# Optimization experiments

Measured on AMD Instinct MI355X. Metric: run time of the kernel, lower is better.

Reference implementation:

```python
import jax, jax.numpy as jnp
import numpy as np
from jax import lax

B, T, H, CTX, CONV_OUT = 32, 1536, 1024, 1024, 32


def setup_inputs() -> dict:
    key = jax.random.key(0)
    ks = jax.random.split(key, 10)
    s = 1.0 / np.sqrt(H)
    return {
        "decoder_output": jax.random.normal(ks[0], (B, 1, H), jnp.float32),
        "encoder_outputs": jax.random.normal(ks[1], (B, T, H), jnp.float32),
        "last_alignment": jax.random.uniform(ks[2], (B, T), jnp.float32),
        "W": jax.random.normal(ks[3], (CTX, H), jnp.float32) * s,
        "V": jax.random.normal(ks[4], (CTX, H), jnp.float32) * s,
        "U": jax.random.normal(ks[5], (CTX, CONV_OUT), jnp.float32) * (1.0 / np.sqrt(CONV_OUT)),
        "b": jax.random.uniform(ks[6], (CTX,), jnp.float32, -0.1, 0.1),
        "w": jax.random.normal(ks[7], (CTX,), jnp.float32) * (1.0 / np.sqrt(CTX)),
        "conv_w": jax.random.normal(ks[8], (CONV_OUT, 1, 3), jnp.float32) * 0.5,
        "conv_b": jax.random.normal(ks[9], (CONV_OUT,), jnp.float32) * 0.1,
    }


def reference(decoder_output, encoder_outputs, last_alignment, W, V, U, b, w, conv_w, conv_b):
    # location feature: Conv1d(1 -> conv_out, k=3, pad=1) over previous alignment
    conv = lax.conv_general_dilated(
        last_alignment[:, None, :], conv_w,
        window_strides=(1,), padding=[(1, 1)],
        dimension_numbers=("NCW", "OIW", "NCW"),
    ) + conv_b[None, :, None]                      # (B, conv_out, T)
    loc = jnp.transpose(conv, (0, 2, 1))           # (B, T, conv_out)

    # additive (Bahdanau) energies: (B,1,ctx) + (B,T,ctx) + (B,T,ctx) + (ctx,)
    e = jnp.tanh(
        jnp.einsum("bqh,ch->bqc", decoder_output, W)
        + jnp.einsum("bth,ch->btc", encoder_outputs, V)
        + jnp.einsum("btk,ck->btc", loc, U)
        + b
    )                                              # (B, T, ctx)
    scores = jnp.einsum("btc,c->bt", e, w)         # (B, T)
    alignment = jax.nn.softmax(scores, axis=-1)    # (B, T)
    context = jnp.einsum("bt,bth->bh", alignment, encoder_outputs)  # (B, H)
    return context, alignment
```

## Files before the change

kernel.cpp:

```cpp
#include <hip/hip_runtime.h>
#include <hip/hip_bf16.h>
#include <hip/hip_fp16.h>


constexpr int kB = 32, kT = 1536, kH = 1024, kC = 1024, kCO = 32;
constexpr int kM = kB * kT;
constexpr int kKp = 1088;

typedef _Float16 f16;
typedef _Float16 f16x8 __attribute__((ext_vector_type(8)));
typedef float f32x4 __attribute__((ext_vector_type(4)));

constexpr size_t W2_A    = 0;
constexpr size_t W2_B    = W2_A + (size_t)kM * kKp * 2;
constexpr size_t W2_ADD  = W2_B + (size_t)kC * kKp * 2;
constexpr size_t W2_SCR  = W2_ADD + (size_t)kB * kC * 4;

__device__ __forceinline__ void gload16(const void* g, void* l) {
    __builtin_amdgcn_global_load_lds(
        (const __attribute__((address_space(1))) void*)g,
        (__attribute__((address_space(3))) void*)l, 16, 0, 0);
}

__global__ void k_cvt(const float* __restrict__ enc, f16* __restrict__ Af) {
    int gid = blockIdx.x * 256 + threadIdx.x;
    int row = gid >> 7, c8 = gid & 127;
    const float* src = enc + (size_t)row * kH + c8 * 8;
    float4 e0 = *(const float4*)src;
    float4 e1 = *(const float4*)(src + 4);
    union { f16 h[8]; int4 q; } u;
    u.h[0] = (f16)e0.x; u.h[1] = (f16)e0.y; u.h[2] = (f16)e0.z; u.h[3] = (f16)e0.w;
    u.h[4] = (f16)e1.x; u.h[5] = (f16)e1.y; u.h[6] = (f16)e1.z; u.h[7] = (f16)e1.w;
    *(int4*)(Af + (size_t)row * kKp + c8 * 8) = u.q;
}

__global__ void k_loc(const float* __restrict__ la, const float* __restrict__ cw,
                      const float* __restrict__ cb, f16* __restrict__ Af) {
    int m = blockIdx.x * 256 + threadIdx.x;
    int b = m / kT, t = m - b * kT;
    float x0 = (t > 0)      ? la[(size_t)b * kT + t - 1] : 0.f;
    float x1 = la[(size_t)b * kT + t];
    float x2 = (t < kT - 1) ? la[(size_t)b * kT + t + 1] : 0.f;
    union { f16 h[32]; int4 q[4]; } u;
#pragma unroll
    for (int k = 0; k < 32; ++k)
        u.h[k] = (f16)(cw[k * 3] * x0 + cw[k * 3 + 1] * x1 + cw[k * 3 + 2] * x2 + cb[k]);
    int4* dst = (int4*)(Af + (size_t)m * kKp + kH);
    dst[0] = u.q[0]; dst[1] = u.q[1]; dst[2] = u.q[2]; dst[3] = u.q[3];
    int4 z = {0, 0, 0, 0};
    dst[4] = z; dst[5] = z; dst[6] = z; dst[7] = z;
}

__global__ void k_prep_b2(const float* __restrict__ V, const float* __restrict__ U,
                          f16* __restrict__ Bf) {
    int c = blockIdx.x, k8 = threadIdx.x;
    if (k8 >= 136) return;
    union { f16 h[8]; int4 q; } u;
    if (k8 < 128) {
        const float* src = V + (size_t)c * kH + k8 * 8;
        float4 a = *(const float4*)src, b = *(const float4*)(src + 4);
        u.h[0] = (f16)a.x; u.h[1] = (f16)a.y; u.h[2] = (f16)a.z; u.h[3] = (f16)a.w;
        u.h[4] = (f16)b.x; u.h[5] = (f16)b.y; u.h[6] = (f16)b.z; u.h[7] = (f16)b.w;
    } else if (k8 < 132) {
        const float* src = U + (size_t)c * kCO + (k8 - 128) * 8;
        float4 a = *(const float4*)src, b = *(const float4*)(src + 4);
        u.h[0] = (f16)a.x; u.h[1] = (f16)a.y; u.h[2] = (f16)a.z; u.h[3] = (f16)a.w;
        u.h[4] = (f16)b.x; u.h[5] = (f16)b.y; u.h[6] = (f16)b.z; u.h[7] = (f16)b.w;
    } else {
        u.q = (int4){0, 0, 0, 0};
    }
    *(int4*)(Bf + (size_t)c * kKp + k8 * 8) = u.q;
}

__global__ void k_prep_add(const float* __restrict__ dec, const float* __restrict__ W,
                           const float* __restrict__ bias, float* __restrict__ add) {
    __shared__ float dl[kH];
    int bb = blockIdx.x >> 2;
    int cc = (blockIdx.x & 3) * 256 + threadIdx.x;
    *(float4*)&dl[threadIdx.x * 4] = *(const float4*)&dec[(size_t)bb * kH + threadIdx.x * 4];
    __syncthreads();
    float acc = bias[cc];
    const float* wr = W + (size_t)cc * kH;
    for (int h = 0; h < kH; h += 4) {
        float4 wv = *(const float4*)&wr[h];
        acc += wv.x * dl[h] + wv.y * dl[h + 1] + wv.z * dl[h + 2] + wv.w * dl[h + 3];
    }
    add[(size_t)bb * kC + cc] = acc;
}

__launch_bounds__(256, 4)
__global__ void k_main(const f16* __restrict__ Ag, const f16* __restrict__ Bg,
                       const float* __restrict__ add, const float* __restrict__ wvec,
                       float* __restrict__ spart) {
    __shared__ __align__(16) char smem[34816];
    float* add_l = (float*)(smem + 32768);
    float* w_l   = (float*)(smem + 33280);
    float (*sred)[64][2] = (float (*)[64][2])(smem + 33792);

    const int tid = threadIdx.x, lane = tid & 63, wave = tid >> 6;
    const int wm = wave >> 1, wn = wave & 1;
    const int raw = blockIdx.x;
    const int lin = (raw & 7) * 384 + (raw >> 3);
    const int mt = lin >> 3, nt = lin & 7;
    const int m0 = mt * 128, n0 = nt * 128;
    const int bb = m0 / kT;

    if (tid < 128) {
        add_l[tid] = add[(size_t)bb * kC + n0 + tid];
        w_l[tid]   = wvec[n0 + tid];
    }

    f32x4 acc[4][4];
#pragma unroll
    for (int i = 0; i < 4; ++i)
#pragma unroll
        for (int j = 0; j < 4; ++j) acc[i][j] = (f32x4){0.f, 0.f, 0.f, 0.f};

    const int SRl  = lane >> 3;
    const int slot = (lane & 7) ^ SRl;
    const int scol = (slot & 3) * 8;
    const int sr0  = 2 * (wave * 16 + SRl) + (slot >> 2);
    const int sr1  = 2 * (wave * 16 + 8 + SRl) + (slot >> 2);
    const f16* aS0 = Ag + (size_t)(m0 + sr0) * kKp + scol;
    const f16* aS1 = Ag + (size_t)(m0 + sr1) * kKp + scol;
    const f16* bS0 = Bg + (size_t)(n0 + sr0) * kKp + scol;
    const f16* bS1 = Bg + (size_t)(n0 + sr1) * kKp + scol;
    const unsigned aDst = wave * 2048u;
    const unsigned bDst = 8192u + wave * 2048u;

    const int g = lane >> 4, rl = lane & 15;
    const unsigned phys = (unsigned)((((rl & 1) << 2) + g) ^ (rl >> 1));
    const unsigned aRd = (unsigned)((wm * 32 + (rl >> 1)) * 128) + phys * 16u;
    const unsigned bRd = 8192u + (unsigned)((wn * 32 + (rl >> 1)) * 128) + phys * 16u;

    gload16(aS0, smem + aDst);
    gload16(aS1, smem + aDst + 1024);
    gload16(bS0, smem + bDst);
    gload16(bS1, smem + bDst + 1024);
    __syncthreads();

    unsigned bufC = 0u;
    for (int t = 0; t < 34; ++t) {
        if (t < 33) {
            const int o = (t + 1) * 32;
            const unsigned bn = bufC ^ 16384u;
            gload16(aS0 + o, smem + bn + aDst);
            gload16(aS1 + o, smem + bn + aDst + 1024);
            gload16(bS0 + o, smem + bn + bDst);
            gload16(bS1 + o, smem + bn + bDst + 1024);
        }
        f16x8 af[4], bfv[4];
#pragma unroll
        for (int ni = 0; ni < 4; ++ni)
            bfv[ni] = *(const f16x8*)(smem + bufC + bRd + ni * 1024);
#pragma unroll
        for (int mi = 0; mi < 4; ++mi)
            af[mi] = *(const f16x8*)(smem + bufC + aRd + mi * 1024);
        __builtin_amdgcn_s_setprio(1);
#pragma unroll
        for (int mi = 0; mi < 4; ++mi)
#pragma unroll
            for (int ni = 0; ni < 4; ++ni)
                acc[mi][ni] = __builtin_amdgcn_mfma_f32_16x16x32_f16(af[mi], bfv[ni], acc[mi][ni], 0, 0, 0);
        __builtin_amdgcn_s_setprio(0);
        __syncthreads();
        bufC ^= 16384u;
    }

#pragma unroll
    for (int mi = 0; mi < 4; ++mi) {
#pragma unroll
        for (int i = 0; i < 4; ++i) {
            float p = 0.f;
#pragma unroll
            for (int ni = 0; ni < 4; ++ni) {
                int cl = wn * 64 + ni * 16 + rl;
                float e = tanhf(acc[mi][ni][i] + add_l[cl]);
                p += e * w_l[cl];
            }
            p += __shfl_xor(p, 1);
            p += __shfl_xor(p, 2);
            p += __shfl_xor(p, 4);
            p += __shfl_xor(p, 8);
            if (rl == 0) sred[wm][mi * 16 + g * 4 + i][wn] = p;
        }
    }
    __syncthreads();
    if (tid < 128) {
        int r = tid & 63, w2 = tid >> 6;
        float s = sred[w2][r][0] + sred[w2][r][1];
        spart[(size_t)nt * kM + m0 + tid] = s;
    }
}

__global__ void k_softmax(const float* __restrict__ spart, float* __restrict__ out_align) {
    __shared__ float red[256];
    int b = blockIdx.x, tid = threadIdx.x;
    float v[6];
    float mx = -1e30f;
#pragma unroll
    for (int i = 0; i < 6; ++i) {
        size_t idx = (size_t)b * kT + tid + i * 256;
        float s = 0.f;
#pragma unroll
        for (int p = 0; p < 8; ++p) s += spart[(size_t)p * kM + idx];
        v[i] = s; mx = fmaxf(mx, s);
    }
    red[tid] = mx; __syncthreads();
    for (int o = 128; o > 0; o >>= 1) { if (tid < o) red[tid] = fmaxf(red[tid], red[tid + o]); __syncthreads(); }
    mx = red[0]; __syncthreads();
    float sum = 0.f;
#pragma unroll
    for (int i = 0; i < 6; ++i) { v[i] = expf(v[i] - mx); sum += v[i]; }
    red[tid] = sum; __syncthreads();
    for (int o = 128; o > 0; o >>= 1) { if (tid < o) red[tid] += red[tid + o]; __syncthreads(); }
    float inv = 1.f / red[0];
#pragma unroll
    for (int i = 0; i < 6; ++i)
        out_align[(size_t)b * kT + tid + i * 256] = v[i] * inv;
}

__global__ void k_ctx_part(const f16* __restrict__ Af, const float* __restrict__ align,
                           float* __restrict__ cpart) {
    __shared__ float al[192];
    int ci = blockIdx.x, b = blockIdx.y, tid = threadIdx.x;
    if (tid < 192) al[tid] = align[(size_t)b * kT + ci * 192 + tid];
    __syncthreads();
    const int half = tid >> 7;
    const int c8 = tid & 127;
    float a0 = 0.f, a1 = 0.f, a2 = 0.f, a3 = 0.f, a4 = 0.f, a5 = 0.f, a6 = 0.f, a7 = 0.f;
    const f16* ep = Af + ((size_t)b * kT + ci * 192 + half * 96) * kKp + c8 * 8;
    for (int t = 0; t < 96; ++t) {
        float a = al[half * 96 + t];
        f16x8 e = *(const f16x8*)(ep + (size_t)t * kKp);
        a0 += a * (float)e[0]; a1 += a * (float)e[1]; a2 += a * (float)e[2]; a3 += a * (float)e[3];
        a4 += a * (float)e[4]; a5 += a * (float)e[5]; a6 += a * (float)e[6]; a7 += a * (float)e[7];
    }
    size_t base = ((size_t)(ci * 2 + half) * kB + b) * kH + (size_t)c8 * 8;
    *(float4*)&cpart[base]     = (float4){a0, a1, a2, a3};
    *(float4*)&cpart[base + 4] = (float4){a4, a5, a6, a7};
}

__global__ void k_ctx_red(const float* __restrict__ cpart, float* __restrict__ out_ctx) {
    int idx = blockIdx.x * 256 + threadIdx.x;
    float s = 0.f;
#pragma unroll
    for (int p = 0; p < 16; ++p) s += cpart[(size_t)p * kB * kH + idx];
    out_ctx[idx] = s;
}

extern "C" void kernel_launch(void* const* d_in, const int* in_sizes, int n_in,
                              void* d_out, int out_size, void* d_ws, size_t ws_size,
                              hipStream_t stream) {
    const float* dec  = (const float*)d_in[0];
    const float* enc  = (const float*)d_in[1];
    const float* la   = (const float*)d_in[2];
    const float* W    = (const float*)d_in[3];
    const float* V    = (const float*)d_in[4];
    const float* U    = (const float*)d_in[5];
    const float* bias = (const float*)d_in[6];
    const float* wv   = (const float*)d_in[7];
    const float* cw   = (const float*)d_in[8];
    const float* cb   = (const float*)d_in[9];

    char* ws = (char*)d_ws;
    f16* Af      = (f16*)(ws + W2_A);
    f16* Bf      = (f16*)(ws + W2_B);
    float* add   = (float*)(ws + W2_ADD);
    float* spart = (float*)(ws + W2_SCR);
    float* cpart = (float*)(ws + W2_SCR);

    float* out_ctx   = (float*)d_out;
    float* out_align = (float*)d_out + kB * kH;

    hipLaunchKernelGGL(k_prep_b2,  dim3(kC),             dim3(256), 0, stream, V, U, Bf);
    hipLaunchKernelGGL(k_loc,      dim3(kM / 256),       dim3(256), 0, stream, la, cw, cb, Af);
    hipLaunchKernelGGL(k_cvt,      dim3(kM * kH / 8 / 256), dim3(256), 0, stream, enc, Af);
    hipLaunchKernelGGL(k_prep_add, dim3(kB * 4),         dim3(256), 0, stream, dec, W, bias, add);
    hipLaunchKernelGGL(k_main,     dim3((kM / 128) * 8), dim3(256), 0, stream, Af, Bf, add, wv, spart);
    hipLaunchKernelGGL(k_softmax,  dim3(kB),             dim3(256), 0, stream, spart, out_align);
    hipLaunchKernelGGL(k_ctx_part, dim3(8, kB),          dim3(256), 0, stream, Af, out_align, cpart);
    hipLaunchKernelGGL(k_ctx_red,  dim3(kB * kH / 256),  dim3(256), 0, stream, cpart, out_ctx);
}
```

Baseline: 254.7 us.

## Load B fragments directly from global and stage only A in single-buffered LDS

The GEMM main loop stops staging the weight (B) tile through LDS and instead has each lane read its MFMA B fragments straight from global memory. The A tile is staged with a wider 64-column K-chunk per sync, using one buffer instead of double buffering, which halves LDS use to raise occupancy. This trades LDS traffic and footprint for more global/L2 loads and removes the load/compute overlap that double buffering gave, so global latency is more exposed per iteration.

```diff
diff --git a/kernel.cpp b/kernel.cpp
--- a/kernel.cpp
+++ b/kernel.cpp
@@ -92,10 +92,10 @@
 __global__ void k_main(const f16* __restrict__ Ag, const f16* __restrict__ Bg,
                        const float* __restrict__ add, const float* __restrict__ wvec,
                        float* __restrict__ spart) {
-    __shared__ __align__(16) char smem[34816];
-    float* add_l = (float*)(smem + 32768);
-    float* w_l   = (float*)(smem + 33280);
-    float (*sred)[64][2] = (float (*)[64][2])(smem + 33792);
+    __shared__ __align__(16) char smem[18432];
+    float* add_l = (float*)(smem + 16384);
+    float* w_l   = (float*)(smem + 16896);
+    float (*sred)[64][2] = (float (*)[64][2])(smem + 17408);
 
     const int tid = threadIdx.x, lane = tid & 63, wave = tid >> 6;
     const int wm = wave >> 1, wn = wave & 1;
@@ -116,56 +116,49 @@
 #pragma unroll
         for (int j = 0; j < 4; ++j) acc[i][j] = (f32x4){0.f, 0.f, 0.f, 0.f};
 
-    const int SRl  = lane >> 3;
-    const int slot = (lane & 7) ^ SRl;
-    const int scol = (slot & 3) * 8;
-    const int sr0  = 2 * (wave * 16 + SRl) + (slot >> 2);
-    const int sr1  = 2 * (wave * 16 + 8 + SRl) + (slot >> 2);
-    const f16* aS0 = Ag + (size_t)(m0 + sr0) * kKp + scol;
-    const f16* aS1 = Ag + (size_t)(m0 + sr1) * kKp + scol;
-    const f16* bS0 = Bg + (size_t)(n0 + sr0) * kKp + scol;
-    const f16* bS1 = Bg + (size_t)(n0 + sr1) * kKp + scol;
-    const unsigned aDst = wave * 2048u;
-    const unsigned bDst = 8192u + wave * 2048u;
+    const int rG = lane >> 3;
+    const int gc = (lane & 7) ^ rG;
+    const f16* aS[4];
+#pragma unroll
+    for (int j = 0; j < 4; ++j)
+        aS[j] = Ag + (size_t)(m0 + wave * 32 + j * 8 + rG) * kKp + gc * 8;
+    const unsigned aDst = wave * 4096u;
 
     const int g = lane >> 4, rl = lane & 15;
-    const unsigned phys = (unsigned)((((rl & 1) << 2) + g) ^ (rl >> 1));
-    const unsigned aRd = (unsigned)((wm * 32 + (rl >> 1)) * 128) + phys * 16u;
-    const unsigned bRd = 8192u + (unsigned)((wn * 32 + (rl >> 1)) * 128) + phys * 16u;
-
-    gload16(aS0, smem + aDst);
-    gload16(aS1, smem + aDst + 1024);
-    gload16(bS0, smem + bDst);
-    gload16(bS1, smem + bDst + 1024);
-    __syncthreads();
-
-    unsigned bufC = 0u;
-    for (int t = 0; t < 34; ++t) {
-        if (t < 33) {
-            const int o = (t + 1) * 32;
-            const unsigned bn = bufC ^ 16384u;
-            gload16(aS0 + o, smem + bn + aDst);
-            gload16(aS1 + o, smem + bn + aDst + 1024);
-            gload16(bS0 + o, smem + bn + bDst);
-            gload16(bS1 + o, smem + bn + bDst + 1024);
-        }
-        f16x8 af[4], bfv[4];
-#pragma unroll
-        for (int ni = 0; ni < 4; ++ni)
-            bfv[ni] = *(const f16x8*)(smem + bufC + bRd + ni * 1024);
-#pragma unroll
-        for (int mi = 0; mi < 4; ++mi)
-            af[mi] = *(const f16x8*)(smem + bufC + aRd + mi * 1024);
-        __builtin_amdgcn_s_setprio(1);
-#pragma unroll
-        for (int mi = 0; mi < 4; ++mi)
-#pragma unroll
-            for (int ni = 0; ni < 4; ++ni)
-                acc[mi][ni] = __builtin_amdgcn_mfma_f32_16x16x32_f16(af[mi], bfv[ni], acc[mi][ni], 0, 0, 0);
-        __builtin_amdgcn_s_setprio(0);
-        __syncthreads();
-        bufC ^= 16384u;
-    }
+    const f16* bP[4];
+#pragma unroll
+    for (int ni = 0; ni < 4; ++ni)
+        bP[ni] = Bg + (size_t)(n0 + wn * 64 + ni * 16 + rl) * kKp + g * 8;
+
+#define KK_STEP(T, KK) {                                                                      \
+    f16x8 bfv[4], af[4];                                                                      \
+    _Pragma("unroll") for (int ni = 0; ni < 4; ++ni)                                          \
+        bfv[ni] = *(const f16x8*)(bP[ni] + (T) * 64 + (KK) * 32);                             \
+    _Pragma("unroll") for (int mi = 0; mi < 4; ++mi)                                          \
+        af[mi] = *(const f16x8*)(smem + (wm * 64 + mi * 16 + rl) * 128                        \
+                                 + ((((KK) * 4 + g) ^ (rl & 7)) << 4));                       \
+    __builtin_amdgcn_s_setprio(1);                                                            \
+    _Pragma("unroll") for (int mi = 0; mi < 4; ++mi)                                          \
+        _Pragma("unroll") for (int ni = 0; ni < 4; ++ni)                                      \
+            acc[mi][ni] = __builtin_amdgcn_mfma_f32_16x16x32_f16(af[mi], bfv[ni], acc[mi][ni], 0, 0, 0); \
+    __builtin_amdgcn_s_setprio(0); }
+
+    for (int t = 0; t < 16; ++t) {
+#pragma unroll
+        for (int j = 0; j < 4; ++j) gload16(aS[j] + t * 64, smem + aDst + j * 1024);
+        __syncthreads();
+        KK_STEP(t, 0)
+        KK_STEP(t, 1)
+        __syncthreads();
+    }
+    {
+#pragma unroll
+        for (int j = 0; j < 4; ++j) gload16(aS[j] + 1024, smem + aDst + j * 1024);
+        __syncthreads();
+        KK_STEP(16, 0)
+        __syncthreads();
+    }
+#undef KK_STEP
 
 #pragma unroll
     for (int mi = 0; mi < 4; ++mi) {
```

Result: slower. 325.1 us (+27.7%).
